# Optimization experiments

Hardware: AMD Instinct MI355X
Metric: run time of the kernel (lower is better)

## Reference

```python
import jax, jax.numpy as jnp
import numpy as np

B, S, F = 2, 2048, 2048
H, D = 16, 128  # F == H * D


def setup_inputs() -> dict:
    key = jax.random.key(0)
    k1, k2, k3 = jax.random.split(key, 3)
    x = jax.random.normal(k1, (B, S, F), dtype=jnp.float32)
    # causal attention mask, broadcast over batch and heads
    mask = jnp.tril(jnp.ones((S, S), dtype=bool))[None, None, :, :]
    init_std = 0.02
    c_attn_kernel = jax.random.normal(k2, (F, 3 * F), dtype=jnp.float32) * init_std
    c_attn_bias = jnp.zeros((3 * F,), dtype=jnp.float32)
    c_proj_kernel = jax.random.normal(k3, (F, F), dtype=jnp.float32) * init_std
    c_proj_bias = jnp.zeros((F,), dtype=jnp.float32)
    return {
        "x": x,
        "mask": mask,
        "c_attn_kernel": c_attn_kernel,
        "c_attn_bias": c_attn_bias,
        "c_proj_kernel": c_proj_kernel,
        "c_proj_bias": c_proj_bias,
    }


def reference(x, mask, c_attn_kernel, c_attn_bias, c_proj_kernel, c_proj_bias):
    dtype = x.dtype
    # fused QKV projection: [B,S,F] @ [F,3F] -> [B,S,3F]
    hidden = jnp.einsum('bsf,fe->bse', x, c_attn_kernel) + c_attn_bias
    q, k, v = jnp.split(hidden, 3, axis=-1)
    split = lambda t: t.reshape(t.shape[:-1] + (H, D))  # [B,S,H,D]
    q, k, v = split(q), split(k), split(v)
    q = q / jnp.sqrt(jnp.asarray(D, dtype))
    scores = jnp.einsum('bqhd,bkhd->bhqk', q, k)  # [B,H,S,S]
    big_neg = jnp.finfo(dtype).min
    scores = jnp.where(mask[..., :S, :S], scores, big_neg)
    weights = jax.nn.softmax(scores, axis=-1)
    z = jnp.einsum('bhqk,bkhd->bqhd', weights, v)  # [B,S,H,D]
    merged = z.reshape(z.shape[:-2] + (F,))  # [B,S,F]
    out = jnp.einsum('bsf,fe->bse', merged, c_proj_kernel) + c_proj_bias
    return out
```

## Files before the change

### kernel.cpp

```cpp
#include <hip/hip_runtime.h>
#include <hip/hip_bf16.h>
#include <stdint.h>

typedef __attribute__((ext_vector_type(8))) __bf16 bf16x8;
typedef __attribute__((ext_vector_type(4))) __bf16 bf16x4;
typedef __attribute__((ext_vector_type(4))) float f32x4;

#define DEV __device__ __forceinline__

static constexpr int S = 2048, F = 2048, H = 16, D = 128;
static constexpr int KDIM = F;
static constexpr float QSCALE = 0.08838834764831845f;

DEV void gll16(const void* g, void* l) {
  __builtin_amdgcn_global_load_lds(
      (const __attribute__((address_space(1))) void*)g,
      (__attribute__((address_space(3))) void*)l, 16, 0, 0);
}

DEV f32x4 mfma16(bf16x8 a, bf16x8 b, f32x4 c) {
  return __builtin_amdgcn_mfma_f32_16x16x32_bf16(a, b, c, 0, 0, 0);
}

extern __shared__ char smem[];

#define QBAR()  __builtin_amdgcn_s_barrier()
#define QLGKM() asm volatile("s_waitcnt lgkmcnt(0)" ::: "memory")
#define QSCB()  __builtin_amdgcn_sched_barrier(0)

__global__ void k_prep(const float* __restrict__ x, __bf16* __restrict__ xb,
                       const float* __restrict__ wa, __bf16* __restrict__ wat,
                       const float* __restrict__ wp, __bf16* __restrict__ wpt) {
  __shared__ float t[64][65];
  const int bid = blockIdx.x;
  if (bid < 8192) {
    int i = bid * 256 + threadIdx.x;
    float4 v = reinterpret_cast<const float4*>(x)[i];
    bf16x4 o = {(__bf16)v.x, (__bf16)v.y, (__bf16)v.z, (__bf16)v.w};
    reinterpret_cast<bf16x4*>(xb)[i] = o;
    return;
  }
  const float* in;
  __bf16* out;
  int rows, cols, c0, r0;
  if (bid < 11264) {
    int tb = bid - 8192;
    in = wa; out = wat; rows = 2048; cols = 6144;
    c0 = (tb % 96) * 64; r0 = (tb / 96) * 64;
  } else {
    int tb = bid - 11264;
    in = wp; out = wpt; rows = 2048; cols = 2048;
    c0 = (tb % 32) * 64; r0 = (tb / 32) * 64;
  }
  const int tx = threadIdx.x & 63, ty = threadIdx.x >> 6;
#pragma unroll
  for (int i = 0; i < 64; i += 4)
    t[ty + i][tx] = in[(size_t)(r0 + ty + i) * cols + c0 + tx];
  __syncthreads();
#pragma unroll
  for (int i = 0; i < 64; i += 4)
    out[(size_t)(c0 + ty + i) * rows + r0 + tx] = (__bf16)t[tx][ty + i];
}

__global__ __launch_bounds__(512, 1) void k_qkv8p(
    const __bf16* __restrict__ A, const __bf16* __restrict__ Bt,
    const float* __restrict__ bias,
    __bf16* __restrict__ qo, __bf16* __restrict__ ko, __bf16* __restrict__ vo) {
  constexpr int NT = 32;
  const int tid = threadIdx.x;
  const int lane = tid & 63, wid = tid >> 6;
  const int wm = wid >> 2, wn = wid & 3;
  const int ln = lane & 15, lm = lane >> 4;

  const int lin = (blockIdx.x & 7) * 64 + (blockIdx.x >> 3);
  const int by = lin >> 4, bx = lin & 15;
  const int mBase = by * 128, nBase = bx * 384;

  const int r0 = tid >> 3, cc = tid & 7;
  const int src0 = r0 * KDIM + ((cc ^ (r0 & 7)) << 3);
  const __bf16* Ab = A + (size_t)mBase * KDIM + src0;
  const __bf16* Bb = Bt + (size_t)nBase * KDIM + src0;
  const int sDst = wid * 1024;

  auto stA2 = [&](int t) {
    char* d = smem + (t & 1) * 65536 + sDst;
    const __bf16* s = Ab + t * 64;
    gll16(s, d);
    gll16(s + (size_t)64 * KDIM, d + 8192);
  };
  auto stB2 = [&](int t, int j) {
    char* d = smem + (t & 1) * 65536 + 16384 + j * 8192 + sDst;
    const __bf16* s = Bb + (size_t)j * 64 * KDIM + t * 64;
    gll16(s, d);
    gll16(s + (size_t)64 * KDIM, d + 8192);
  };

  int rA[2], rB[2];
#pragma unroll
  for (int ks = 0; ks < 2; ++ks) {
    const int slot = (ks * 4 + lm) ^ (ln & 7);
    rA[ks] = (wm * 64 + ln) * 128 + slot * 16;
    rB[ks] = 16384 + (wn * 96 + ln) * 128 + slot * 16;
  }
  auto rdA = [&](bf16x8 (&a)[4], const char* cb, int ks) {
#pragma unroll
    for (int mi = 0; mi < 4; ++mi)
      a[mi] = *reinterpret_cast<const bf16x8*>(cb + rA[ks] + mi * 2048);
  };
  auto rdBh = [&](bf16x8 (&b)[3], const char* cb, int ks, int h) {
#pragma unroll
    for (int k = 0; k < 3; ++k)
      b[k] = *reinterpret_cast<const bf16x8*>(cb + rB[ks] + (h * 3 + k) * 2048);
  };

  f32x4 acc[4][6] = {};
  auto mm = [&](const bf16x8 (&a)[4], const bf16x8 (&b)[3], int h) {
#pragma unroll
    for (int k = 0; k < 3; ++k)
#pragma unroll
      for (int mi = 0; mi < 4; ++mi)
        acc[mi][h * 3 + k] = mfma16(a[mi], b[k], acc[mi][h * 3 + k]);
  };

  stA2(0); stB2(0, 0); stB2(0, 2); stB2(0, 4); stA2(1);
  asm volatile("s_waitcnt vmcnt(2)" ::: "memory");
  QBAR(); QSCB();

  for (int i = 0; i < 16; ++i) {
    const char* L = smem;
    const char* R = smem + 65536;
    const int tR = 2 * i + 1, tN = 2 * i + 2, tN1 = 2 * i + 3;
    const bool last = (i == 15);
    bf16x8 a[4], b[3];

    rdA(a, L, 0); rdBh(b, L, 0, 0);
    stB2(tR, 0);
    QBAR(); QLGKM(); QSCB();
    __builtin_amdgcn_s_setprio(1); mm(a, b, 0); __builtin_amdgcn_s_setprio(0);
    QBAR(); QSCB();

    rdBh(b, L, 0, 1);
    stB2(tR, 2);
    QBAR(); QLGKM(); QSCB();
    __builtin_amdgcn_s_setprio(1); mm(a, b, 1); __builtin_amdgcn_s_setprio(0);
    QBAR(); QSCB();

    rdA(a, L, 1); rdBh(b, L, 1, 1);
    stB2(tR, 4);
    QBAR(); QLGKM(); QSCB();
    __builtin_amdgcn_s_setprio(1); mm(a, b, 1); __builtin_amdgcn_s_setprio(0);
    QBAR(); QSCB();

    rdBh(b, L, 1, 0);
    if (!last) stA2(tN);
    QBAR(); QLGKM(); QSCB();
    __builtin_amdgcn_s_setprio(1); mm(a, b, 0); __builtin_amdgcn_s_setprio(0);
    if (last) asm volatile("s_waitcnt vmcnt(0)" ::: "memory");
    else      asm volatile("s_waitcnt vmcnt(2)" ::: "memory");
    QBAR(); QSCB();

    rdA(a, R, 0); rdBh(b, R, 0, 0);
    if (!last) stB2(tN, 0);
    QBAR(); QLGKM(); QSCB();
    __builtin_amdgcn_s_setprio(1); mm(a, b, 0); __builtin_amdgcn_s_setprio(0);
    QBAR(); QSCB();

    rdBh(b, R, 0, 1);
    if (!last) stB2(tN, 2);
    QBAR(); QLGKM(); QSCB();
    __builtin_amdgcn_s_setprio(1); mm(a, b, 1); __builtin_amdgcn_s_setprio(0);
    QBAR(); QSCB();

    rdA(a, R, 1); rdBh(b, R, 1, 1);
    if (!last) stB2(tN, 4);
    QBAR(); QLGKM(); QSCB();
    __builtin_amdgcn_s_setprio(1); mm(a, b, 1); __builtin_amdgcn_s_setprio(0);
    QBAR(); QSCB();

    rdBh(b, R, 1, 0);
    if (tN1 < NT) stA2(tN1);
    QBAR(); QLGKM(); QSCB();
    __builtin_amdgcn_s_setprio(1); mm(a, b, 0); __builtin_amdgcn_s_setprio(0);
    if (!last) {
      asm volatile("s_waitcnt vmcnt(2)" ::: "memory");
      QBAR(); QSCB();
    }
  }

#pragma unroll
  for (int mi = 0; mi < 4; ++mi) {
    const int grow = mBase + wm * 64 + mi * 16 + lm * 4;
    const int b = grow >> 11, s0 = grow & 2047;
#pragma unroll
    for (int ni = 0; ni < 6; ++ni) {
      const int gcol = nBase + wn * 96 + ni * 16 + ln;
      const float bv = bias[gcol];
      const int sec = gcol >> 11;
      const int h = (gcol >> 7) & 15, d = gcol & 127;
      const int bh = b * H + h;
      if (sec == 0) {
#pragma unroll
        for (int r = 0; r < 4; ++r)
          qo[((size_t)bh * S + s0 + r) * D + d] = (__bf16)((acc[mi][ni][r] + bv) * QSCALE);
      } else if (sec == 1) {
#pragma unroll
        for (int r = 0; r < 4; ++r)
          ko[((size_t)bh * S + s0 + r) * D + d] = (__bf16)(acc[mi][ni][r] + bv);
      } else {
        bf16x4 pv = {(__bf16)(acc[mi][ni][0] + bv), (__bf16)(acc[mi][ni][1] + bv),
                     (__bf16)(acc[mi][ni][2] + bv), (__bf16)(acc[mi][ni][3] + bv)};
        *reinterpret_cast<bf16x4*>(vo + ((size_t)bh * D + d) * S + s0) = pv;
      }
    }
  }
}

__global__ __launch_bounds__(512, 1) void k_proj8p(
    const __bf16* __restrict__ A, const __bf16* __restrict__ Bt,
    const float* __restrict__ bias, float* __restrict__ fo) {
  constexpr int NT = 32;
  const int tid = threadIdx.x;
  const int lane = tid & 63, wid = tid >> 6;
  const int wm = wid >> 2, wn = wid & 3;
  const int ln = lane & 15, lm = lane >> 4;

  const int lin = (blockIdx.x & 7) * 32 + (blockIdx.x >> 3);
  const int by = lin >> 3, bx = lin & 7;
  const int mBase = by * 128, nBase = bx * 256;

  const int r0 = tid >> 3, cc = tid & 7;
  const int src0 = r0 * KDIM + ((cc ^ (r0 & 7)) << 3);
  const __bf16* Ab = A + (size_t)mBase * KDIM + src0;
  const __bf16* Bb = Bt + (size_t)nBase * KDIM + src0;
  const int sDst = wid * 1024;

  auto stA2 = [&](int t) {
    char* d = smem + (t & 1) * 49152 + sDst;
    const __bf16* s = Ab + t * 64;
    gll16(s, d);
    gll16(s + (size_t)64 * KDIM, d + 8192);
  };
  auto stB2 = [&](int t, int j) {
    char* d = smem + (t & 1) * 49152 + 16384 + j * 8192 + sDst;
    const __bf16* s = Bb + (size_t)j * 64 * KDIM + t * 64;
    gll16(s, d);
    gll16(s + (size_t)64 * KDIM, d + 8192);
  };

  int rA[2], rB[2];
#pragma unroll
  for (int ks = 0; ks < 2; ++ks) {
    const int slot = (ks * 4 + lm) ^ (ln & 7);
    rA[ks] = (wm * 64 + ln) * 128 + slot * 16;
    rB[ks] = 16384 + (wn * 64 + ln) * 128 + slot * 16;
  }
  auto rdA = [&](bf16x8 (&a)[4], const char* cb, int ks) {
#pragma unroll
    for (int mi = 0; mi < 4; ++mi)
      a[mi] = *reinterpret_cast<const bf16x8*>(cb + rA[ks] + mi * 2048);
  };
  auto rdBh = [&](bf16x8 (&b)[2], const char* cb, int ks, int h) {
#pragma unroll
    for (int k = 0; k < 2; ++k)
      b[k] = *reinterpret_cast<const bf16x8*>(cb + rB[ks] + (h * 2 + k) * 2048);
  };

  f32x4 acc[4][4] = {};
  auto mm = [&](const bf16x8 (&a)[4], const bf16x8 (&b)[2], int h) {
#pragma unroll
    for (int k = 0; k < 2; ++k)
#pragma unroll
      for (int mi = 0; mi < 4; ++mi)
        acc[mi][h * 2 + k] = mfma16(a[mi], b[k], acc[mi][h * 2 + k]);
  };

  stA2(0); stB2(0, 0); stB2(0, 2); stA2(1);
  asm volatile("s_waitcnt vmcnt(2)" ::: "memory");
  QBAR(); QSCB();

  for (int i = 0; i < 16; ++i) {
    const char* L = smem;
    const char* R = smem + 49152;
    const int tR = 2 * i + 1, tN = 2 * i + 2, tN1 = 2 * i + 3;
    const bool last = (i == 15);
    bf16x8 a[4], b[2];

    rdA(a, L, 0); rdBh(b, L, 0, 0);
    stB2(tR, 0);
    QBAR(); QLGKM(); QSCB();
    __builtin_amdgcn_s_setprio(1); mm(a, b, 0); __builtin_amdgcn_s_setprio(0);
    QBAR(); QSCB();
    rdBh(b, L, 0, 1);
    stB2(tR, 2);
    QBAR(); QLGKM(); QSCB();
    __builtin_amdgcn_s_setprio(1); mm(a, b, 1); __builtin_amdgcn_s_setprio(0);
    QBAR(); QSCB();
    rdA(a, L, 1); rdBh(b, L, 1, 1);
    if (!last) stA2(tN);
    QBAR(); QLGKM(); QSCB();
    __builtin_amdgcn_s_setprio(1); mm(a, b, 1); __builtin_amdgcn_s_setprio(0);
    QBAR(); QSCB();
    rdBh(b, L, 1, 0);
    QBAR(); QLGKM(); QSCB();
    __builtin_amdgcn_s_setprio(1); mm(a, b, 0); __builtin_amdgcn_s_setprio(0);
    if (last) asm volatile("s_waitcnt vmcnt(0)" ::: "memory");
    else      asm volatile("s_waitcnt vmcnt(2)" ::: "memory");
    QBAR(); QSCB();

    rdA(a, R, 0); rdBh(b, R, 0, 0);
    if (!last) stB2(tN, 0);
    QBAR(); QLGKM(); QSCB();
    __builtin_amdgcn_s_setprio(1); mm(a, b, 0); __builtin_amdgcn_s_setprio(0);
    QBAR(); QSCB();
    rdBh(b, R, 0, 1);
    if (!last) stB2(tN, 2);
    QBAR(); QLGKM(); QSCB();
    __builtin_amdgcn_s_setprio(1); mm(a, b, 1); __builtin_amdgcn_s_setprio(0);
    QBAR(); QSCB();
    rdA(a, R, 1); rdBh(b, R, 1, 1);
    if (tN1 < NT) stA2(tN1);
    QBAR(); QLGKM(); QSCB();
    __builtin_amdgcn_s_setprio(1); mm(a, b, 1); __builtin_amdgcn_s_setprio(0);
    QBAR(); QSCB();
    rdBh(b, R, 1, 0);
    QBAR(); QLGKM(); QSCB();
    __builtin_amdgcn_s_setprio(1); mm(a, b, 0); __builtin_amdgcn_s_setprio(0);
    if (!last) {
      asm volatile("s_waitcnt vmcnt(2)" ::: "memory");
      QBAR(); QSCB();
    }
  }

#pragma unroll
  for (int mi = 0; mi < 4; ++mi) {
    const int grow = mBase + wm * 64 + mi * 16 + lm * 4;
#pragma unroll
    for (int ni = 0; ni < 4; ++ni) {
      const int gcol = nBase + wn * 64 + ni * 16 + ln;
      const float bv = bias[gcol];
#pragma unroll
      for (int r = 0; r < 4; ++r)
        fo[(size_t)(grow + r) * F + gcol] = acc[mi][ni][r] + bv;
    }
  }
}

__global__ __launch_bounds__(256, 2) void k_attn(
    const __bf16* __restrict__ qb, const __bf16* __restrict__ kb,
    const __bf16* __restrict__ vtb, __bf16* __restrict__ zb) {
  const int lane = threadIdx.x & 63, w = threadIdx.x >> 6;
  const int lm = lane >> 4, ln = lane & 15;
  const int blk = blockIdx.x;
  const int u = blk & 255, v = blk >> 8;
  const int qt = v ? (u >> 4) : 15 - (u >> 4);
  const int bh = ((u & 15) << 1) | v;
  const int qw = qt * 128 + w * 32;

  const __bf16* qp = qb + (size_t)bh * S * D;
  const __bf16* kp = kb + (size_t)bh * S * D;
  const __bf16* vp = vtb + (size_t)bh * D * S;
  char* pw = smem + 65536 + w * 4096;

  int ksrc[4], kdst[4], vsrc[4], vdst[4];
#pragma unroll
  for (int j = 0; j < 4; ++j) {
    int c = (w * 4 + j) * 64 + lane;
    int kr = c >> 4, kps = (c & 15) ^ (kr & 7);
    ksrc[j] = kr * D + kps * 8;
    kdst[j] = (w * 4 + j) * 1024;
    int vr = c >> 3, vps = (c & 7) ^ (vr & 7);
    vsrc[j] = vr * S + vps * 8;
    vdst[j] = 16384 + (w * 4 + j) * 1024;
  }
  auto stage = [&](int kt) {
    char* buf = smem + (kt & 1) * 32768;
    const int kv = kt * 64;
#pragma unroll
    for (int j = 0; j < 4; ++j) gll16(kp + (size_t)kv * D + ksrc[j], buf + kdst[j]);
#pragma unroll
    for (int j = 0; j < 4; ++j) gll16(vp + kv + vsrc[j], buf + vdst[j]);
  };

  bf16x8 qf[2][4];
#pragma unroll
  for (int mi = 0; mi < 2; ++mi)
#pragma unroll
    for (int kf = 0; kf < 4; ++kf)
      qf[mi][kf] = *reinterpret_cast<const bf16x8*>(qp + (qw + mi * 16 + ln) * D + kf * 32 + lm * 8);

  f32x4 Oa[2][8] = {};
  float mrow[2][4], lrow[2][4];
#pragma unroll
  for (int mi = 0; mi < 2; ++mi)
#pragma unroll
    for (int r = 0; r < 4; ++r) { mrow[mi][r] = -3.0e38f; lrow[mi][r] = 0.0f; }

  const int ktEnd = 2 * qt + 1;

  stage(0);
  stage(1);
  asm volatile("s_waitcnt vmcnt(8)" ::: "memory");
  QBAR(); QSCB();

  for (int kt = 0; kt <= ktEnd; ++kt) {
    const int kv0 = kt * 64;
    const int cur = kt & 1;
    const char* Kb = smem + cur * 32768;
    const char* Vb = Kb + 16384;

    if (kv0 <= qw + 31) {
      const bool diag = (kv0 + 63 > qw);

      f32x4 sacc[2][4] = {};
#pragma unroll
      for (int kf = 0; kf < 4; ++kf) {
        bf16x8 kfr[4];
#pragma unroll
        for (int ni = 0; ni < 4; ++ni) {
          int row = ni * 16 + ln;
          int ch = (kf * 4 + lm) ^ (row & 7);
          kfr[ni] = *reinterpret_cast<const bf16x8*>(Kb + row * 256 + ch * 16);
        }
        __builtin_amdgcn_s_setprio(1);
#pragma unroll
        for (int mi = 0; mi < 2; ++mi)
#pragma unroll
          for (int ni = 0; ni < 4; ++ni)
            sacc[mi][ni] = mfma16(qf[mi][kf], kfr[ni], sacc[mi][ni]);
        __builtin_amdgcn_s_setprio(0);
      }

      if (diag) {
#pragma unroll
        for (int ni = 0; ni < 4; ++ni) {
          int c = kv0 + ni * 16 + ln;
#pragma unroll
          for (int mi = 0; mi < 2; ++mi) {
            int q0r = qw + mi * 16 + lm * 4;
#pragma unroll
            for (int r = 0; r < 4; ++r)
              if (c > q0r + r) sacc[mi][ni][r] = -1e30f;
          }
        }
      }

      float lmax[2][4];
      bool big = false;
#pragma unroll
      for (int mi = 0; mi < 2; ++mi)
#pragma unroll
        for (int r = 0; r < 4; ++r) {
          float m4 = fmaxf(fmaxf(sacc[mi][0][r], sacc[mi][1][r]),
                           fmaxf(sacc[mi][2][r], sacc[mi][3][r]));
          lmax[mi][r] = m4;
          big = big || (m4 > mrow[mi][r] + 8.0f);
        }
      if (__any((int)big)) {
#pragma unroll
        for (int mi = 0; mi < 2; ++mi)
#pragma unroll
          for (int r = 0; r < 4; ++r) {
            float mx = lmax[mi][r];
            mx = fmaxf(mx, __shfl_xor(mx, 1, 64));
            mx = fmaxf(mx, __shfl_xor(mx, 2, 64));
            mx = fmaxf(mx, __shfl_xor(mx, 4, 64));
            mx = fmaxf(mx, __shfl_xor(mx, 8, 64));
            float mnew = fmaxf(mrow[mi][r], mx);
            float corr = __expf(mrow[mi][r] - mnew);
            mrow[mi][r] = mnew;
            lrow[mi][r] *= corr;
#pragma unroll
            for (int ni = 0; ni < 8; ++ni) Oa[mi][ni][r] *= corr;
          }
      }
#pragma unroll
      for (int mi = 0; mi < 2; ++mi)
#pragma unroll
        for (int r = 0; r < 4; ++r) {
          float rs = 0.0f;
#pragma unroll
          for (int ni = 0; ni < 4; ++ni) {
            float p = __expf(sacc[mi][ni][r] - mrow[mi][r]);
            sacc[mi][ni][r] = p;
            rs += p;
          }
          lrow[mi][r] += rs;
        }

#pragma unroll
      for (int mi = 0; mi < 2; ++mi)
#pragma unroll
        for (int ni = 0; ni < 4; ++ni)
#pragma unroll
          for (int r = 0; r < 4; ++r) {
            int row = mi * 16 + lm * 4 + r;
            int bo = (row * 128 + (ni * 16 + ln) * 2) ^ ((row & 7) << 4);
            *reinterpret_cast<__bf16*>(pw + bo) = (__bf16)sacc[mi][ni][r];
          }

      QLGKM(); QSCB();

#pragma unroll
      for (int kf = 0; kf < 2; ++kf) {
        bf16x8 pfr[2], vfr[8];
#pragma unroll
        for (int mi = 0; mi < 2; ++mi) {
          int row = mi * 16 + ln;
          int ch = (kf * 4 + lm) ^ (row & 7);
          pfr[mi] = *reinterpret_cast<const bf16x8*>(pw + row * 128 + ch * 16);
        }
#pragma unroll
        for (int ni = 0; ni < 8; ++ni) {
          int row = ni * 16 + ln;
          int ch = (kf * 4 + lm) ^ (row & 7);
          vfr[ni] = *reinterpret_cast<const bf16x8*>(Vb + row * 128 + ch * 16);
        }
        __builtin_amdgcn_s_setprio(1);
#pragma unroll
        for (int mi = 0; mi < 2; ++mi)
#pragma unroll
          for (int ni = 0; ni < 8; ++ni)
            Oa[mi][ni] = mfma16(pfr[mi], vfr[ni], Oa[mi][ni]);
        __builtin_amdgcn_s_setprio(0);
      }
    }

    asm volatile("s_waitcnt lgkmcnt(0)" ::: "memory");
    QBAR(); QSCB();
    if (kt + 2 <= ktEnd) stage(kt + 2);
    if (kt + 1 <= ktEnd) {
      if (kt + 2 <= ktEnd)
        asm volatile("s_waitcnt vmcnt(8)" ::: "memory");
      else
        asm volatile("s_waitcnt vmcnt(0)" ::: "memory");
      QBAR(); QSCB();
    }
  }

#pragma unroll
  for (int mi = 0; mi < 2; ++mi)
#pragma unroll
    for (int r = 0; r < 4; ++r) {
      float ls = lrow[mi][r];
      ls += __shfl_xor(ls, 1, 64);
      ls += __shfl_xor(ls, 2, 64);
      ls += __shfl_xor(ls, 4, 64);
      ls += __shfl_xor(ls, 8, 64);
      lrow[mi][r] = 1.0f / ls;
    }
  const int b = bh >> 4, h = bh & 15;
#pragma unroll
  for (int mi = 0; mi < 2; ++mi)
#pragma unroll
    for (int ni = 0; ni < 8; ++ni) {
      int d = ni * 16 + ln;
#pragma unroll
      for (int r = 0; r < 4; ++r) {
        int qrow = qw + mi * 16 + lm * 4 + r;
        zb[(size_t)(b * S + qrow) * F + h * D + d] = (__bf16)(Oa[mi][ni][r] * lrow[mi][r]);
      }
    }
}

extern "C" void kernel_launch(void* const* d_in, const int* in_sizes, int n_in,
                              void* d_out, int out_size, void* d_ws, size_t ws_size,
                              hipStream_t stream) {
  const float* x = (const float*)d_in[0];
  const float* w_attn = (const float*)d_in[2];
  const float* b_attn = (const float*)d_in[3];
  const float* w_proj = (const float*)d_in[4];
  const float* b_proj = (const float*)d_in[5];
  float* out = (float*)d_out;

  char* ws = (char*)d_ws;
  __bf16* xb    = (__bf16*)(ws + 0);
  __bf16* wqkv  = (__bf16*)(ws + 16777216);
  __bf16* wpro  = (__bf16*)(ws + 41943040);
  __bf16* qb    = (__bf16*)(ws + 50331648);
  __bf16* kb    = (__bf16*)(ws + 67108864);
  __bf16* vtb   = (__bf16*)(ws + 83886080);
  __bf16* zb    = xb;

  (void)hipFuncSetAttribute((const void*)k_qkv8p,
                            hipFuncAttributeMaxDynamicSharedMemorySize, 131072);
  (void)hipFuncSetAttribute((const void*)k_proj8p,
                            hipFuncAttributeMaxDynamicSharedMemorySize, 98304);
  (void)hipFuncSetAttribute((const void*)k_attn,
                            hipFuncAttributeMaxDynamicSharedMemorySize, 81920);

  k_prep<<<12288, 256, 0, stream>>>(x, xb, w_attn, wqkv, w_proj, wpro);
  k_qkv8p<<<512, 512, 131072, stream>>>(xb, wqkv, b_attn, qb, kb, vtb);
  k_attn<<<512, 256, 81920, stream>>>(qb, kb, vtb, zb);
  k_proj8p<<<256, 512, 98304, stream>>>(zb, wpro, b_proj, out);
}
```

Measured before the change: 233.4 us.

## Transpose attention MFMA operands so each lane owns a query row

The QK^T and PV MFMAs now swap operand order, computing S^T and O^T so that each lane holds one query row across its accumulator registers. Row max and row sum reductions now work mostly within registers and need only two cross-lane shuffles instead of four per row. Stores of P to LDS and of the output Z become 4-wide bf16 vector stores instead of scalar 2-byte stores. This reduces shuffle, softmax bookkeeping and store instruction counts, but changes the LDS write pattern and swizzle, which could shift bank conflicts.

```diff
diff --git a/kernel.cpp b/kernel.cpp
--- a/kernel.cpp
+++ b/kernel.cpp
@@ -290,16 +290,19 @@
     QBAR(); QLGKM(); QSCB();
     __builtin_amdgcn_s_setprio(1); mm(a, b, 0); __builtin_amdgcn_s_setprio(0);
     QBAR(); QSCB();
+
     rdBh(b, L, 0, 1);
     stB2(tR, 2);
     QBAR(); QLGKM(); QSCB();
     __builtin_amdgcn_s_setprio(1); mm(a, b, 1); __builtin_amdgcn_s_setprio(0);
     QBAR(); QSCB();
+
     rdA(a, L, 1); rdBh(b, L, 1, 1);
     if (!last) stA2(tN);
     QBAR(); QLGKM(); QSCB();
     __builtin_amdgcn_s_setprio(1); mm(a, b, 1); __builtin_amdgcn_s_setprio(0);
     QBAR(); QSCB();
+
     rdBh(b, L, 1, 0);
     QBAR(); QLGKM(); QSCB();
     __builtin_amdgcn_s_setprio(1); mm(a, b, 0); __builtin_amdgcn_s_setprio(0);
@@ -312,16 +315,19 @@
     QBAR(); QLGKM(); QSCB();
     __builtin_amdgcn_s_setprio(1); mm(a, b, 0); __builtin_amdgcn_s_setprio(0);
     QBAR(); QSCB();
+
     rdBh(b, R, 0, 1);
     if (!last) stB2(tN, 2);
     QBAR(); QLGKM(); QSCB();
     __builtin_amdgcn_s_setprio(1); mm(a, b, 1); __builtin_amdgcn_s_setprio(0);
     QBAR(); QSCB();
+
     rdA(a, R, 1); rdBh(b, R, 1, 1);
     if (tN1 < NT) stA2(tN1);
     QBAR(); QLGKM(); QSCB();
     __builtin_amdgcn_s_setprio(1); mm(a, b, 1); __builtin_amdgcn_s_setprio(0);
     QBAR(); QSCB();
+
     rdBh(b, R, 1, 0);
     QBAR(); QLGKM(); QSCB();
     __builtin_amdgcn_s_setprio(1); mm(a, b, 0); __builtin_amdgcn_s_setprio(0);
@@ -383,17 +389,15 @@
 
   bf16x8 qf[2][4];
 #pragma unroll
-  for (int mi = 0; mi < 2; ++mi)
+  for (int nj = 0; nj < 2; ++nj)
 #pragma unroll
     for (int kf = 0; kf < 4; ++kf)
-      qf[mi][kf] = *reinterpret_cast<const bf16x8*>(qp + (qw + mi * 16 + ln) * D + kf * 32 + lm * 8);
-
-  f32x4 Oa[2][8] = {};
-  float mrow[2][4], lrow[2][4];
-#pragma unroll
-  for (int mi = 0; mi < 2; ++mi)
-#pragma unroll
-    for (int r = 0; r < 4; ++r) { mrow[mi][r] = -3.0e38f; lrow[mi][r] = 0.0f; }
+      qf[nj][kf] = *reinterpret_cast<const bf16x8*>(qp + (qw + nj * 16 + ln) * D + kf * 32 + lm * 8);
+
+  f32x4 Oa[8][2] = {};
+  float mrow[2], lrow[2];
+#pragma unroll
+  for (int nj = 0; nj < 2; ++nj) { mrow[nj] = -3.0e38f; lrow[nj] = 0.0f; }
 
   const int ktEnd = 2 * qt + 1;
 
@@ -411,92 +415,93 @@
     if (kv0 <= qw + 31) {
       const bool diag = (kv0 + 63 > qw);
 
-      f32x4 sacc[2][4] = {};
+      f32x4 sacc[4][2] = {};
 #pragma unroll
       for (int kf = 0; kf < 4; ++kf) {
         bf16x8 kfr[4];
 #pragma unroll
-        for (int ni = 0; ni < 4; ++ni) {
-          int row = ni * 16 + ln;
+        for (int mi = 0; mi < 4; ++mi) {
+          int row = mi * 16 + ln;
           int ch = (kf * 4 + lm) ^ (row & 7);
-          kfr[ni] = *reinterpret_cast<const bf16x8*>(Kb + row * 256 + ch * 16);
+          kfr[mi] = *reinterpret_cast<const bf16x8*>(Kb + row * 256 + ch * 16);
         }
         __builtin_amdgcn_s_setprio(1);
 #pragma unroll
-        for (int mi = 0; mi < 2; ++mi)
-#pragma unroll
-          for (int ni = 0; ni < 4; ++ni)
-            sacc[mi][ni] = mfma16(qf[mi][kf], kfr[ni], sacc[mi][ni]);
+        for (int mi = 0; mi < 4; ++mi)
+#pragma unroll
+          for (int nj = 0; nj < 2; ++nj)
+            sacc[mi][nj] = mfma16(kfr[mi], qf[nj][kf], sacc[mi][nj]);
         __builtin_amdgcn_s_setprio(0);
       }
 
       if (diag) {
 #pragma unroll
-        for (int ni = 0; ni < 4; ++ni) {
-          int c = kv0 + ni * 16 + ln;
-#pragma unroll
-          for (int mi = 0; mi < 2; ++mi) {
-            int q0r = qw + mi * 16 + lm * 4;
+        for (int nj = 0; nj < 2; ++nj) {
+          int q = qw + nj * 16 + ln;
+#pragma unroll
+          for (int mi = 0; mi < 4; ++mi) {
+            int kvb = kv0 + mi * 16 + lm * 4;
 #pragma unroll
             for (int r = 0; r < 4; ++r)
-              if (c > q0r + r) sacc[mi][ni][r] = -1e30f;
+              if (kvb + r > q) sacc[mi][nj][r] = -1e30f;
           }
         }
       }
 
-      float lmax[2][4];
+      float lmax[2];
       bool big = false;
 #pragma unroll
-      for (int mi = 0; mi < 2; ++mi)
-#pragma unroll
-        for (int r = 0; r < 4; ++r) {
-          float m4 = fmaxf(fmaxf(sacc[mi][0][r], sacc[mi][1][r]),
-                           fmaxf(sacc[mi][2][r], sacc[mi][3][r]));
-          lmax[mi][r] = m4;
-          big = big || (m4 > mrow[mi][r] + 8.0f);
+      for (int nj = 0; nj < 2; ++nj) {
+        float m4 = -3.0e38f;
+#pragma unroll
+        for (int mi = 0; mi < 4; ++mi)
+#pragma unroll
+          for (int r = 0; r < 4; ++r) m4 = fmaxf(m4, sacc[mi][nj][r]);
+        lmax[nj] = m4;
+        big = big || (m4 > mrow[nj] + 8.0f);
+      }
+      if (__any((int)big)) {
+#pragma unroll
+        for (int nj = 0; nj < 2; ++nj) {
+          float mx = lmax[nj];
+          mx = fmaxf(mx, __shfl_xor(mx, 16, 64));
+          mx = fmaxf(mx, __shfl_xor(mx, 32, 64));
+          float mnew = fmaxf(mrow[nj], mx);
+          float corr = __expf(mrow[nj] - mnew);
+          mrow[nj] = mnew;
+          lrow[nj] *= corr;
+#pragma unroll
+          for (int ni = 0; ni < 8; ++ni)
+#pragma unroll
+            for (int r = 0; r < 4; ++r) Oa[ni][nj][r] *= corr;
         }
-      if (__any((int)big)) {
-#pragma unroll
-        for (int mi = 0; mi < 2; ++mi)
+      }
+#pragma unroll
+      for (int nj = 0; nj < 2; ++nj) {
+        float rs = 0.0f;
+#pragma unroll
+        for (int mi = 0; mi < 4; ++mi)
 #pragma unroll
           for (int r = 0; r < 4; ++r) {
-            float mx = lmax[mi][r];
-            mx = fmaxf(mx, __shfl_xor(mx, 1, 64));
-            mx = fmaxf(mx, __shfl_xor(mx, 2, 64));
-            mx = fmaxf(mx, __shfl_xor(mx, 4, 64));
-            mx = fmaxf(mx, __shfl_xor(mx, 8, 64));
-            float mnew = fmaxf(mrow[mi][r], mx);
-            float corr = __expf(mrow[mi][r] - mnew);
-            mrow[mi][r] = mnew;
-            lrow[mi][r] *= corr;
-#pragma unroll
-            for (int ni = 0; ni < 8; ++ni) Oa[mi][ni][r] *= corr;
-          }
-      }
-#pragma unroll
-      for (int mi = 0; mi < 2; ++mi)
-#pragma unroll
-        for (int r = 0; r < 4; ++r) {
-          float rs = 0.0f;
-#pragma unroll
-          for (int ni = 0; ni < 4; ++ni) {
-            float p = __expf(sacc[mi][ni][r] - mrow[mi][r]);
-            sacc[mi][ni][r] = p;
+            float p = __expf(sacc[mi][nj][r] - mrow[nj]);
+            sacc[mi][nj][r] = p;
             rs += p;
           }
-          lrow[mi][r] += rs;
+        lrow[nj] += rs;
+      }
+
+#pragma unroll
+      for (int nj = 0; nj < 2; ++nj) {
+        int row = nj * 16 + ln;
+        int rb = row * 128;
+        int swz = (row & 7) << 4;
+#pragma unroll
+        for (int mi = 0; mi < 4; ++mi) {
+          bf16x4 pq = {(__bf16)sacc[mi][nj][0], (__bf16)sacc[mi][nj][1],
+                       (__bf16)sacc[mi][nj][2], (__bf16)sacc[mi][nj][3]};
+          *reinterpret_cast<bf16x4*>(pw + rb + ((mi * 32 + lm * 8) ^ swz)) = pq;
         }
-
-#pragma unroll
-      for (int mi = 0; mi < 2; ++mi)
-#pragma unroll
-        for (int ni = 0; ni < 4; ++ni)
-#pragma unroll
-          for (int r = 0; r < 4; ++r) {
-            int row = mi * 16 + lm * 4 + r;
-            int bo = (row * 128 + (ni * 16 + ln) * 2) ^ ((row & 7) << 4);
-            *reinterpret_cast<__bf16*>(pw + bo) = (__bf16)sacc[mi][ni][r];
-          }
+      }
 
       QLGKM(); QSCB();
 
@@ -504,10 +509,10 @@
       for (int kf = 0; kf < 2; ++kf) {
         bf16x8 pfr[2], vfr[8];
 #pragma unroll
-        for (int mi = 0; mi < 2; ++mi) {
-          int row = mi * 16 + ln;
-          int ch = (kf * 4 + lm) ^ (row & 7);
-          pfr[mi] = *reinterpret_cast<const bf16x8*>(pw + row * 128 + ch * 16);
+        for (int nj = 0; nj < 2; ++nj) {
+          int row = nj * 16 + ln;
+          pfr[nj] = *reinterpret_cast<const bf16x8*>(
+              pw + row * 128 + ((kf * 64 + lm * 16) ^ ((row & 7) << 4)));
         }
 #pragma unroll
         for (int ni = 0; ni < 8; ++ni) {
@@ -517,10 +522,10 @@
         }
         __builtin_amdgcn_s_setprio(1);
 #pragma unroll
-        for (int mi = 0; mi < 2; ++mi)
-#pragma unroll
-          for (int ni = 0; ni < 8; ++ni)
-            Oa[mi][ni] = mfma16(pfr[mi], vfr[ni], Oa[mi][ni]);
+        for (int ni = 0; ni < 8; ++ni)
+#pragma unroll
+          for (int nj = 0; nj < 2; ++nj)
+            Oa[ni][nj] = mfma16(vfr[ni], pfr[nj], Oa[ni][nj]);
         __builtin_amdgcn_s_setprio(0);
       }
     }
@@ -538,28 +543,24 @@
   }
 
 #pragma unroll
-  for (int mi = 0; mi < 2; ++mi)
-#pragma unroll
-    for (int r = 0; r < 4; ++r) {
-      float ls = lrow[mi][r];
-      ls += __shfl_xor(ls, 1, 64);
-      ls += __shfl_xor(ls, 2, 64);
-      ls += __shfl_xor(ls, 4, 64);
-      ls += __shfl_xor(ls, 8, 64);
-      lrow[mi][r] = 1.0f / ls;
-    }
+  for (int nj = 0; nj < 2; ++nj) {
+    float ls = lrow[nj];
+    ls += __shfl_xor(ls, 16, 64);
+    ls += __shfl_xor(ls, 32, 64);
+    lrow[nj] = 1.0f / ls;
+  }
   const int b = bh >> 4, h = bh & 15;
 #pragma unroll
-  for (int mi = 0; mi < 2; ++mi)
+  for (int nj = 0; nj < 2; ++nj) {
+    const int qrow = qw + nj * 16 + ln;
+    __bf16* zrow = zb + (size_t)(b * S + qrow) * F + h * D + lm * 4;
 #pragma unroll
     for (int ni = 0; ni < 8; ++ni) {
-      int d = ni * 16 + ln;
-#pragma unroll
-      for (int r = 0; r < 4; ++r) {
-        int qrow = qw + mi * 16 + lm * 4 + r;
-        zb[(size_t)(b * S + qrow) * F + h * D + d] = (__bf16)(Oa[mi][ni][r] * lrow[mi][r]);
-      }
-    }
+      bf16x4 oq = {(__bf16)(Oa[ni][nj][0] * lrow[nj]), (__bf16)(Oa[ni][nj][1] * lrow[nj]),
+                   (__bf16)(Oa[ni][nj][2] * lrow[nj]), (__bf16)(Oa[ni][nj][3] * lrow[nj])};
+      *reinterpret_cast<bf16x4*>(zrow + ni * 16) = oq;
+    }
+  }
 }
 
 extern "C" void kernel_launch(void* const* d_in, const int* in_sizes, int n_in,
```

New measurement: 224.3 us, median of 2. 1.04x faster.
